# Kernel tuning notes

Measured on AMD Instinct MI355X. Metric: run time of the kernel, lower is better.

Reference implementation:

```python
import jax, jax.numpy as jnp
import numpy as np

N_FEAT = 512
N_HIDDEN = 512


def setup_inputs() -> dict:
    key = jax.random.key(0)
    ks = jax.random.split(key, 8)
    B, T, F = 32, 2048, N_FEAT
    H = N_HIDDEN
    s_ih = 1.0 / np.sqrt(H)
    X = jax.random.normal(ks[0], (B, T, F), dtype=jnp.float32)
    # PyTorch LSTMCell params: weight_ih [4H, F], weight_hh [4H, H], biases [4H]
    W_ih = jax.random.uniform(ks[1], (4 * H, F), minval=-s_ih, maxval=s_ih, dtype=jnp.float32)
    W_hh = jax.random.uniform(ks[2], (4 * H, H), minval=-s_ih, maxval=s_ih, dtype=jnp.float32)
    b_ih = jax.random.uniform(ks[3], (4 * H,), minval=-s_ih, maxval=s_ih, dtype=jnp.float32)
    b_hh = jax.random.uniform(ks[4], (4 * H,), minval=-s_ih, maxval=s_ih, dtype=jnp.float32)
    s_l = 1.0 / np.sqrt(F)
    W_hs = jax.random.uniform(ks[5], (F, F), minval=-s_l, maxval=s_l, dtype=jnp.float32)
    W_cs = jax.random.uniform(ks[6], (F, F), minval=-s_l, maxval=s_l, dtype=jnp.float32)
    return {"X": X, "W_ih": W_ih, "W_hh": W_hh, "b_ih": b_ih, "b_hh": b_hh,
            "W_hs": W_hs, "W_cs": W_cs}


def reference(X, W_ih, W_hh, b_ih, b_hh, W_hs, W_cs):
    B, T, F = X.shape
    H = W_hh.shape[1]

    def step(carry, xi):
        h, c = carry  # [B, H] each; note: h,c were linearly transformed last step
        gates = xi @ W_ih.T + b_ih + h @ W_hh.T + b_hh  # [B, 4H]
        i_g, f_g, g_g, o_g = jnp.split(gates, 4, axis=-1)  # PyTorch i,f,g,o order
        c_new = jax.nn.sigmoid(f_g) * c + jax.nn.sigmoid(i_g) * jnp.tanh(g_g)
        h_new = jax.nn.sigmoid(o_g) * jnp.tanh(c_new)
        h2 = h_new @ W_hs.T  # hs_state(h)
        c2 = c_new @ W_cs.T  # cs_state(c)
        att = jnp.tanh(h2 + c2)
        out = jnp.tanh(att + xi)
        return (h2, c2), out

    h0 = jnp.zeros((B, H), dtype=X.dtype)
    c0 = jnp.zeros((B, H), dtype=X.dtype)
    _, outs = jax.lax.scan(step, (h0, c0), jnp.transpose(X, (1, 0, 2)))  # [T, B, F]
    outs = jnp.transpose(outs, (1, 0, 2))  # [B, T, F]
    return X + jnp.tanh(outs)
```

## Files before the change

kernel.cpp:

```cpp
#include <hip/hip_runtime.h>

#define T_   2048
#define NWG  32

typedef float  float4v __attribute__((ext_vector_type(4)));
typedef float  float2v __attribute__((ext_vector_type(2)));
typedef short  short8v __attribute__((ext_vector_type(8)));
typedef short  short4v __attribute__((ext_vector_type(4)));
typedef unsigned uint4v __attribute__((ext_vector_type(4)));
typedef unsigned short ushort_t;

__device__ __forceinline__ ushort_t f2bf(float f) {
  union { float f; unsigned u; } v; v.f = f;
  unsigned r = (v.u + 0x7FFFu + ((v.u >> 16) & 1u)) >> 16;
  return (ushort_t)r;
}
__device__ __forceinline__ float bf2f(short s) {
  union { unsigned u; float f; } v; v.u = ((unsigned)(unsigned short)s) << 16;
  return v.f;
}
__device__ __forceinline__ float sigm(float x) {
  x = fmaxf(x, -30.f);
  return __fdividef(1.f, 1.f + __expf(-x));
}
__device__ __forceinline__ float tanh_(float x) {
  x = fminf(fmaxf(x, -15.f), 15.f);
  float e = __expf(2.f * x);
  return (e - 1.f) * __fdividef(1.f, e + 1.f);
}

__device__ __forceinline__ short8v ld_coh16(const ushort_t* p) {
  short8v r;
  asm volatile("global_load_dwordx4 %0, %1, off sc0 sc1" : "=v"(r) : "v"(p));
  return r;
}

__global__ void k_prep_w1(const float* __restrict__ Whh, const float* __restrict__ Whs,
                          ushort_t* __restrict__ w1) {
  int idx = blockIdx.x * 256 + threadIdx.x;
  if (idx >= 2048 * 512) return;
  int n = idx >> 9, k = idx & 511;
  const float* whr = Whh + (size_t)n * 512;
  const float* wsk = Whs + k;
  float s = 0.f;
  #pragma unroll 8
  for (int j = 0; j < 512; ++j) s += whr[j] * wsk[(size_t)j * 512];
  w1[idx] = f2bf(s);
}

__global__ void k_prep_misc(const float* __restrict__ Wih, const float* __restrict__ Wcs,
                            const float* __restrict__ Whs, const float* __restrict__ bih,
                            const float* __restrict__ bhh,
                            ushort_t* __restrict__ wih_bf, ushort_t* __restrict__ wcs_bf,
                            ushort_t* __restrict__ whs_bf, float* __restrict__ bias,
                            ushort_t* __restrict__ HN, ushort_t* __restrict__ CN,
                            int* __restrict__ flags) {
  const int total = 1048576 + 262144 + 262144 + 2048 + 16384 + 16384 + 512;
  for (int i = blockIdx.x * blockDim.x + threadIdx.x; i < total; i += gridDim.x * blockDim.x) {
    int r = i;
    if (r < 1048576) { wih_bf[r] = f2bf(Wih[r]); continue; }
    r -= 1048576;
    if (r < 262144)  { wcs_bf[r] = f2bf(Wcs[r]); continue; }
    r -= 262144;
    if (r < 262144)  { whs_bf[r] = f2bf(Whs[r]); continue; }
    r -= 262144;
    if (r < 2048)    { bias[r] = bih[r] + bhh[r]; continue; }
    r -= 2048;
    if (r < 16384)   { HN[3 * 16384 + r] = 0; continue; }
    r -= 16384;
    if (r < 16384)   { CN[3 * 16384 + r] = 0; continue; }
    r -= 16384;
    flags[r] = 0;
  }
}

__global__ __launch_bounds__(256) void k_gemm_g(
    const float* __restrict__ X, const ushort_t* __restrict__ wih,
    ushort_t* __restrict__ G) {
  const int bid = blockIdx.x;
  const int fb  = bid & 31;
  const int tg  = bid >> 5;
  const int wid = threadIdx.x >> 6;
  const int lane = threadIdx.x & 63;
  const int t   = tg * 4 + wid;
  const int ar  = lane & 15;
  const int ko  = (lane >> 4) << 3;

  float4v acc[2][4];
  #pragma unroll
  for (int mh = 0; mh < 2; ++mh)
    #pragma unroll
    for (int cg = 0; cg < 4; ++cg)
      acc[mh][cg] = float4v{0.f, 0.f, 0.f, 0.f};

  #pragma unroll 4
  for (int kk = 0; kk < 16; ++kk) {
    short8v a[2];
    #pragma unroll
    for (int mh = 0; mh < 2; ++mh) {
      const float* p = X + (size_t)(mh * 16 + ar) * (T_ * 512) + (size_t)t * 512 + kk * 32 + ko;
      float4v xa = *(const float4v*)(p);
      float4v xb = *(const float4v*)(p + 4);
      uint4v ua = __builtin_bit_cast(uint4v, xa);
      uint4v ub = __builtin_bit_cast(uint4v, xb);
      uint4v pk;
      pk[0] = __builtin_amdgcn_perm(ua[1], ua[0], 0x07060302u);
      pk[1] = __builtin_amdgcn_perm(ua[3], ua[2], 0x07060302u);
      pk[2] = __builtin_amdgcn_perm(ub[1], ub[0], 0x07060302u);
      pk[3] = __builtin_amdgcn_perm(ub[3], ub[2], 0x07060302u);
      a[mh] = __builtin_bit_cast(short8v, pk);
    }
    #pragma unroll
    for (int cg = 0; cg < 4; ++cg) {
      short8v b = *(const short8v*)(wih + ((size_t)(cg * 512 + fb * 16 + ar)) * 512 + kk * 32 + ko);
      acc[0][cg] = __builtin_amdgcn_mfma_f32_16x16x32_bf16(a[0], b, acc[0][cg], 0, 0, 0);
      acc[1][cg] = __builtin_amdgcn_mfma_f32_16x16x32_bf16(a[1], b, acc[1][cg], 0, 0, 0);
    }
  }

  const size_t base = ((size_t)t * 32 + fb) * 2048;
  #pragma unroll
  for (int mh = 0; mh < 2; ++mh)
    #pragma unroll
    for (int cg = 0; cg < 4; ++cg) {
      short4v s;
      #pragma unroll
      for (int r = 0; r < 4; ++r) s[r] = (short)f2bf(acc[mh][cg][r]);
      *(short4v*)(G + base + cg * 512 + ar * 32 + mh * 16 + ((lane >> 4) << 2)) = s;
    }
}

__global__ __launch_bounds__(256, 1) void k_lstm_pre(
    const float* __restrict__ X,
    const ushort_t* __restrict__ w1,
    const ushort_t* __restrict__ wcs, const ushort_t* __restrict__ whs,
    const float* __restrict__ bias, const ushort_t* __restrict__ G,
    ushort_t* __restrict__ HN, ushort_t* __restrict__ CN,
    int* __restrict__ flags, float* __restrict__ out)
{
  const int fb   = blockIdx.x;
  const int tid  = threadIdx.x;
  const int wid  = tid >> 6;
  const int lane = tid & 63;
  const int mh   = wid & 1;
  const int ar   = lane & 15;
  const int ko   = (lane >> 4) << 3;

  __shared__ float s_tiles[12][16][20];

  const int eb  = tid >> 3;
  const int ejp = (tid & 7) * 2;
  const int emh = eb >> 4, ebr = eb & 15;
  float bI[2], bF[2], bG[2], bO[2];
  #pragma unroll
  for (int u = 0; u < 2; ++u) {
    bI[u] = bias[0 * 512 + fb * 16 + ejp + u];
    bF[u] = bias[1 * 512 + fb * 16 + ejp + u];
    bG[u] = bias[2 * 512 + fb * 16 + ejp + u];
    bO[u] = bias[3 * 512 + fb * 16 + ejp + u];
  }

  const int gtype0 = wid >> 1;
  const int gtype1 = 2 + (wid >> 1);

  short8v bw0[16], bw1[16], bw2[16];
  {
    const ushort_t* p0 = w1 + ((size_t)(gtype0 * 512 + fb * 16 + ar)) * 512 + ko;
    const ushort_t* p1 = w1 + ((size_t)(gtype1 * 512 + fb * 16 + ar)) * 512 + ko;
    const ushort_t* p2 = ((wid < 2) ? wcs : whs) + ((size_t)(fb * 16 + ar)) * 512 + ko;
    #pragma unroll
    for (int kk = 0; kk < 16; ++kk) {
      bw0[kk] = *(const short8v*)(p0 + (size_t)kk * 32);
      bw1[kk] = *(const short8v*)(p1 + (size_t)kk * 32);
      bw2[kk] = *(const short8v*)(p2 + (size_t)kk * 32);
    }
  }

  const int arow_x = mh * 16 + ar;
  const int t0 = wid, t1 = wid + 4, t2 = wid + 8;
  const int glo = ((lane >> 4) << 2) + mh * 16 + ar * 32;

  short4v gp0, gp1;
  {
    const ushort_t* gb = G + (size_t)fb * 2048 + glo;
    gp0 = *(const short4v*)(gb + gtype0 * 512);
    gp1 = *(const short4v*)(gb + gtype1 * 512);
  }

  for (int t = 0; t <= T_; ++t) {
    float2v xo2 = {0.f, 0.f};
    if (t > 0)
      xo2 = *(const float2v*)&X[(size_t)eb * (T_ * 512) + (size_t)(t - 1) * 512 + fb * 16 + ejp];

    if (t > 0) {
      while (true) {
        int v = (lane < NWG)
              ? __hip_atomic_load(flags + lane * 16, __ATOMIC_RELAXED, __HIP_MEMORY_SCOPE_AGENT)
              : t;
        if (__all(v >= t)) break;
      }
      __builtin_amdgcn_sched_barrier(0);
    }

    const int rs = (t + 3) & 3;
    const ushort_t* hb = HN + (size_t)rs * (32 * 512) + (size_t)arow_x * 512 + ko;
    short8v hfrag[16];
    #pragma unroll
    for (int kk = 0; kk < 16; ++kk)
      hfrag[kk] = ld_coh16(hb + (size_t)kk * 32);
    short8v cfrag[16];
    if (wid < 2) {
      const ushort_t* cb = CN + (size_t)rs * (32 * 512) + (size_t)arow_x * 512 + ko;
      #pragma unroll
      for (int kk = 0; kk < 16; ++kk)
        cfrag[kk] = ld_coh16(cb + (size_t)kk * 32);
    }

    float4v acc0, acc1, acc2;
    #pragma unroll
    for (int r = 0; r < 4; ++r) {
      acc0[r] = bf2f(gp0[r]);
      acc1[r] = bf2f(gp1[r]);
      acc2[r] = 0.f;
    }

    asm volatile("s_waitcnt vmcnt(0)" ::: "memory");
    __builtin_amdgcn_sched_barrier(0);

    #pragma unroll
    for (int kk = 0; kk < 16; ++kk) {
      acc0 = __builtin_amdgcn_mfma_f32_16x16x32_bf16(hfrag[kk], bw0[kk], acc0, 0, 0, 0);
      acc1 = __builtin_amdgcn_mfma_f32_16x16x32_bf16(hfrag[kk], bw1[kk], acc1, 0, 0, 0);
      short8v a2 = (wid < 2) ? cfrag[kk] : hfrag[kk];
      acc2 = __builtin_amdgcn_mfma_f32_16x16x32_bf16(a2, bw2[kk], acc2, 0, 0, 0);
    }

    __syncthreads();

    {
      const int rb = (lane >> 4) << 2, cc = lane & 15;
      #pragma unroll
      for (int r = 0; r < 4; ++r) {
        s_tiles[t0][rb + r][cc] = acc0[r];
        s_tiles[t1][rb + r][cc] = acc1[r];
        s_tiles[t2][rb + r][cc] = acc2[r];
      }
    }
    __syncthreads();

    if (t < T_) {
      unsigned hpk = 0, cpk = 0;
      #pragma unroll
      for (int u = 0; u < 2; ++u) {
        int j = ejp + u;
        float iv  = s_tiles[0 + emh][ebr][j] + bI[u];
        float fv  = s_tiles[2 + emh][ebr][j] + bF[u];
        float gv  = s_tiles[4 + emh][ebr][j] + bG[u];
        float ov  = s_tiles[6 + emh][ebr][j] + bO[u];
        float c2p = s_tiles[8 + emh][ebr][j];
        float cnv = sigm(fv) * c2p + sigm(iv) * tanh_(gv);
        float hnv = sigm(ov) * tanh_(cnv);
        hpk |= ((unsigned)f2bf(hnv)) << (16 * u);
        cpk |= ((unsigned)f2bf(cnv)) << (16 * u);
      }
      size_t uso = (size_t)(t & 3) * (32 * 512) + (size_t)eb * 512 + fb * 16 + ejp;
      __hip_atomic_store((unsigned*)(HN + uso), hpk,
                         __ATOMIC_RELAXED, __HIP_MEMORY_SCOPE_AGENT);
      __hip_atomic_store((unsigned*)(CN + uso), cpk,
                         __ATOMIC_RELAXED, __HIP_MEMORY_SCOPE_AGENT);
    }
    __syncthreads();
    if (t < T_ && tid == 0)
      __hip_atomic_store(flags + fb * 16, t + 1, __ATOMIC_RELAXED, __HIP_MEMORY_SCOPE_AGENT);

    if (t + 1 < T_) {
      const ushort_t* gb = G + ((size_t)((t + 1) * 32 + fb)) * 2048 + glo;
      gp0 = *(const short4v*)(gb + gtype0 * 512);
      gp1 = *(const short4v*)(gb + gtype1 * 512);
    }

    if (t > 0) {
      float ov2[2];
      #pragma unroll
      for (int u = 0; u < 2; ++u) {
        int j = ejp + u;
        float c2p = s_tiles[8 + emh][ebr][j];
        float h2p = s_tiles[10 + emh][ebr][j];
        float att = tanh_(h2p + c2p);
        float xo  = (u ? xo2[1] : xo2[0]);
        float o1  = tanh_(att + xo);
        ov2[u] = xo + tanh_(o1);
      }
      float2v o2; o2[0] = ov2[0]; o2[1] = ov2[1];
      *(float2v*)&out[(size_t)eb * (T_ * 512) + (size_t)(t - 1) * 512 + fb * 16 + ejp] = o2;
    }
  }
}

__global__ __launch_bounds__(256, 1) void k_lstm_fb(
    const float* __restrict__ X,
    const ushort_t* __restrict__ w1, const ushort_t* __restrict__ wih,
    const ushort_t* __restrict__ wcs, const ushort_t* __restrict__ whs,
    const float* __restrict__ bias,
    ushort_t* __restrict__ HN, ushort_t* __restrict__ CN,
    int* __restrict__ flags, float* __restrict__ out)
{
  const int fb   = blockIdx.x;
  const int tid  = threadIdx.x;
  const int wid  = tid >> 6;
  const int lane = tid & 63;
  const int mh   = wid & 1;
  const int ar   = lane & 15;
  const int ko   = (lane >> 4) << 3;

  __shared__ float s_tiles[12][16][20];

  const int eb  = tid >> 3;
  const int ejp = (tid & 7) * 2;
  const int emh = eb >> 4, ebr = eb & 15;
  float bI[2], bF[2], bG[2], bO[2];
  #pragma unroll
  for (int u = 0; u < 2; ++u) {
    bI[u] = bias[0 * 512 + fb * 16 + ejp + u];
    bF[u] = bias[1 * 512 + fb * 16 + ejp + u];
    bG[u] = bias[2 * 512 + fb * 16 + ejp + u];
    bO[u] = bias[3 * 512 + fb * 16 + ejp + u];
  }

  const int gtype0 = wid >> 1;
  const int gtype1 = 2 + (wid >> 1);

  short8v bw0[16], bw1[16], bw2[16];
  {
    const ushort_t* p0 = w1 + ((size_t)(gtype0 * 512 + fb * 16 + ar)) * 512 + ko;
    const ushort_t* p1 = w1 + ((size_t)(gtype1 * 512 + fb * 16 + ar)) * 512 + ko;
    const ushort_t* p2 = ((wid < 2) ? wcs : whs) + ((size_t)(fb * 16 + ar)) * 512 + ko;
    #pragma unroll
    for (int kk = 0; kk < 16; ++kk) {
      bw0[kk] = *(const short8v*)(p0 + (size_t)kk * 32);
      bw1[kk] = *(const short8v*)(p1 + (size_t)kk * 32);
      bw2[kk] = *(const short8v*)(p2 + (size_t)kk * 32);
    }
  }

  const ushort_t* bx0_ = wih + ((size_t)(gtype0 * 512 + fb * 16 + ar)) * 512 + ko;
  const ushort_t* bx1_ = wih + ((size_t)(gtype1 * 512 + fb * 16 + ar)) * 512 + ko;
  const int arow_x = mh * 16 + ar;
  const int t0 = wid, t1 = wid + 4, t2 = wid + 8;

  for (int t = 0; t <= T_; ++t) {
    float4v acc0 = {0.f, 0.f, 0.f, 0.f};
    float4v acc1 = acc0, acc2 = acc0;

    float2v xo2 = {0.f, 0.f};
    if (t > 0)
      xo2 = *(const float2v*)&X[(size_t)eb * (T_ * 512) + (size_t)(t - 1) * 512 + fb * 16 + ejp];

    if (t < T_) {
      const float* xrow = X + (size_t)arow_x * (T_ * 512) + (size_t)t * 512 + ko;
      const ushort_t* bx0 = bx0_;
      const ushort_t* bx1 = bx1_;
      asm volatile("" : "+v"(bx0), "+v"(bx1));
      #pragma unroll
      for (int kk = 0; kk < 16; ++kk) {
        const float* p = xrow + kk * 32;
        float4v xa = *(const float4v*)(p);
        float4v xb = *(const float4v*)(p + 4);
        uint4v ua = __builtin_bit_cast(uint4v, xa);
        uint4v ub = __builtin_bit_cast(uint4v, xb);
        uint4v pk;
        pk[0] = __builtin_amdgcn_perm(ua[1], ua[0], 0x07060302u);
        pk[1] = __builtin_amdgcn_perm(ua[3], ua[2], 0x07060302u);
        pk[2] = __builtin_amdgcn_perm(ub[1], ub[0], 0x07060302u);
        pk[3] = __builtin_amdgcn_perm(ub[3], ub[2], 0x07060302u);
        short8v a = __builtin_bit_cast(short8v, pk);
        short8v b0 = *(const short8v*)(bx0 + (size_t)kk * 32);
        short8v b1 = *(const short8v*)(bx1 + (size_t)kk * 32);
        acc0 = __builtin_amdgcn_mfma_f32_16x16x32_bf16(a, b0, acc0, 0, 0, 0);
        acc1 = __builtin_amdgcn_mfma_f32_16x16x32_bf16(a, b1, acc1, 0, 0, 0);
      }
    }

    if (t > 0) {
      while (true) {
        int v = (lane < NWG)
              ? __hip_atomic_load(flags + lane * 16, __ATOMIC_RELAXED, __HIP_MEMORY_SCOPE_AGENT)
              : t;
        if (__all(v >= t)) break;
      }
      __builtin_amdgcn_sched_barrier(0);
    }

    const int rs = (t + 3) & 3;
    const ushort_t* hb = HN + (size_t)rs * (32 * 512) + (size_t)arow_x * 512 + ko;
    short8v hfrag[16];
    #pragma unroll
    for (int kk = 0; kk < 16; ++kk)
      hfrag[kk] = ld_coh16(hb + (size_t)kk * 32);
    short8v cfrag[16];
    if (wid < 2) {
      const ushort_t* cb = CN + (size_t)rs * (32 * 512) + (size_t)arow_x * 512 + ko;
      #pragma unroll
      for (int kk = 0; kk < 16; ++kk)
        cfrag[kk] = ld_coh16(cb + (size_t)kk * 32);
    }
    asm volatile("s_waitcnt vmcnt(0)" ::: "memory");
    __builtin_amdgcn_sched_barrier(0);

    #pragma unroll
    for (int kk = 0; kk < 16; ++kk) {
      acc0 = __builtin_amdgcn_mfma_f32_16x16x32_bf16(hfrag[kk], bw0[kk], acc0, 0, 0, 0);
      acc1 = __builtin_amdgcn_mfma_f32_16x16x32_bf16(hfrag[kk], bw1[kk], acc1, 0, 0, 0);
      short8v a2 = (wid < 2) ? cfrag[kk] : hfrag[kk];
      acc2 = __builtin_amdgcn_mfma_f32_16x16x32_bf16(a2, bw2[kk], acc2, 0, 0, 0);
    }

    __syncthreads();

    {
      const int rb = (lane >> 4) << 2, cc = lane & 15;
      #pragma unroll
      for (int r = 0; r < 4; ++r) {
        s_tiles[t0][rb + r][cc] = acc0[r];
        s_tiles[t1][rb + r][cc] = acc1[r];
        s_tiles[t2][rb + r][cc] = acc2[r];
      }
    }
    __syncthreads();

    if (t < T_) {
      unsigned hpk = 0, cpk = 0;
      #pragma unroll
      for (int u = 0; u < 2; ++u) {
        int j = ejp + u;
        float iv  = s_tiles[0 + emh][ebr][j] + bI[u];
        float fv  = s_tiles[2 + emh][ebr][j] + bF[u];
        float gv  = s_tiles[4 + emh][ebr][j] + bG[u];
        float ov  = s_tiles[6 + emh][ebr][j] + bO[u];
        float c2p = s_tiles[8 + emh][ebr][j];
        float cnv = sigm(fv) * c2p + sigm(iv) * tanh_(gv);
        float hnv = sigm(ov) * tanh_(cnv);
        hpk |= ((unsigned)f2bf(hnv)) << (16 * u);
        cpk |= ((unsigned)f2bf(cnv)) << (16 * u);
      }
      size_t uso = (size_t)(t & 3) * (32 * 512) + (size_t)eb * 512 + fb * 16 + ejp;
      __hip_atomic_store((unsigned*)(HN + uso), hpk,
                         __ATOMIC_RELAXED, __HIP_MEMORY_SCOPE_AGENT);
      __hip_atomic_store((unsigned*)(CN + uso), cpk,
                         __ATOMIC_RELAXED, __HIP_MEMORY_SCOPE_AGENT);
    }
    __syncthreads();
    if (t < T_ && tid == 0)
      __hip_atomic_store(flags + fb * 16, t + 1, __ATOMIC_RELAXED, __HIP_MEMORY_SCOPE_AGENT);

    if (t > 0) {
      float ov2[2];
      #pragma unroll
      for (int u = 0; u < 2; ++u) {
        int j = ejp + u;
        float c2p = s_tiles[8 + emh][ebr][j];
        float h2p = s_tiles[10 + emh][ebr][j];
        float att = tanh_(h2p + c2p);
        float xo  = (u ? xo2[1] : xo2[0]);
        float o1  = tanh_(att + xo);
        ov2[u] = xo + tanh_(o1);
      }
      float2v o2; o2[0] = ov2[0]; o2[1] = ov2[1];
      *(float2v*)&out[(size_t)eb * (T_ * 512) + (size_t)(t - 1) * 512 + fb * 16 + ejp] = o2;
    }
  }
}

extern "C" void kernel_launch(void* const* d_in, const int* in_sizes, int n_in,
                              void* d_out, int out_size, void* d_ws, size_t ws_size,
                              hipStream_t stream) {
  const float* X   = (const float*)d_in[0];
  const float* Wih = (const float*)d_in[1];
  const float* Whh = (const float*)d_in[2];
  const float* bih = (const float*)d_in[3];
  const float* bhh = (const float*)d_in[4];
  const float* Whs = (const float*)d_in[5];
  const float* Wcs = (const float*)d_in[6];

  char* ws = (char*)d_ws;
  ushort_t* w1_bf  = (ushort_t*)(ws + 0);
  ushort_t* wih_bf = (ushort_t*)(ws + 2097152);
  ushort_t* wcs_bf = (ushort_t*)(ws + 4194304);
  ushort_t* whs_bf = (ushort_t*)(ws + 4718592);
  float*    bias   = (float*)   (ws + 5242880);
  ushort_t* HN     = (ushort_t*)(ws + 5251072);
  ushort_t* CN     = (ushort_t*)(ws + 5382144);
  int*      flags  = (int*)     (ws + 5513216);
  ushort_t* G      = (ushort_t*)(ws + 5515264);
  if (ws_size < (size_t)5515264) return;
  const bool pre = ws_size >= (size_t)5515264 + (size_t)268435456;

  k_prep_w1<<<4096, 256, 0, stream>>>(Whh, Whs, w1_bf);
  k_prep_misc<<<2048, 256, 0, stream>>>(Wih, Wcs, Whs, bih, bhh,
                                        wih_bf, wcs_bf, whs_bf, bias, HN, CN, flags);
  if (pre) {
    k_gemm_g<<<16384, 256, 0, stream>>>(X, wih_bf, G);
    k_lstm_pre<<<NWG, 256, 0, stream>>>(X, w1_bf, wcs_bf, whs_bf, bias, G,
                                        HN, CN, flags, (float*)d_out);
  } else {
    k_lstm_fb<<<NWG, 256, 0, stream>>>(X, w1_bf, wih_bf, wcs_bf, whs_bf, bias,
                                       HN, CN, flags, (float*)d_out);
  }
}
```

Measured before the change: 11.45 ms.

## Double-buffer LDS tiles and replace block barrier with per-wave counter signaling

The shared-memory gate tiles are double-buffered by step parity. This removes two __syncthreads per timestep, and the output epilogue for step t-2 moves into the window before the MFMAs so it overlaps the recurrent-state load latency. The per-workgroup flag written by thread 0 after a block barrier becomes an atomic counter that each wave increments once its own h/c stores have drained. Consumers wait for 4*t arrivals. This shortens the critical path between steps, at the cost of more atomics and an extra epilogue after the loop.

```diff
diff --git a/kernel.cpp b/kernel.cpp
--- a/kernel.cpp
+++ b/kernel.cpp
@@ -54,7 +54,7 @@
                             ushort_t* __restrict__ wih_bf, ushort_t* __restrict__ wcs_bf,
                             ushort_t* __restrict__ whs_bf, float* __restrict__ bias,
                             ushort_t* __restrict__ HN, ushort_t* __restrict__ CN,
-                            int* __restrict__ flags) {
+                            int* __restrict__ cnt) {
   const int total = 1048576 + 262144 + 262144 + 2048 + 16384 + 16384 + 512;
   for (int i = blockIdx.x * blockDim.x + threadIdx.x; i < total; i += gridDim.x * blockDim.x) {
     int r = i;
@@ -70,7 +70,7 @@
     r -= 16384;
     if (r < 16384)   { CN[3 * 16384 + r] = 0; continue; }
     r -= 16384;
-    flags[r] = 0;
+    cnt[r] = 0;
   }
 }
 
@@ -136,7 +136,7 @@
     const ushort_t* __restrict__ wcs, const ushort_t* __restrict__ whs,
     const float* __restrict__ bias, const ushort_t* __restrict__ G,
     ushort_t* __restrict__ HN, ushort_t* __restrict__ CN,
-    int* __restrict__ flags, float* __restrict__ out)
+    int* __restrict__ cnt, float* __restrict__ out)
 {
   const int fb   = blockIdx.x;
   const int tid  = threadIdx.x;
@@ -146,7 +146,7 @@
   const int ar   = lane & 15;
   const int ko   = (lane >> 4) << 3;
 
-  __shared__ float s_tiles[12][16][20];
+  __shared__ float s_tiles[2][12][16][20];
 
   const int eb  = tid >> 3;
   const int ejp = (tid & 7) * 2;
@@ -189,15 +189,16 @@
 
   for (int t = 0; t <= T_; ++t) {
     float2v xo2 = {0.f, 0.f};
-    if (t > 0)
-      xo2 = *(const float2v*)&X[(size_t)eb * (T_ * 512) + (size_t)(t - 1) * 512 + fb * 16 + ejp];
+    if (t >= 2)
+      xo2 = *(const float2v*)&X[(size_t)eb * (T_ * 512) + (size_t)(t - 2) * 512 + fb * 16 + ejp];
 
     if (t > 0) {
+      const int thr = t << 2;
       while (true) {
         int v = (lane < NWG)
-              ? __hip_atomic_load(flags + lane * 16, __ATOMIC_RELAXED, __HIP_MEMORY_SCOPE_AGENT)
-              : t;
-        if (__all(v >= t)) break;
+              ? __hip_atomic_load(cnt + lane * 16, __ATOMIC_RELAXED, __HIP_MEMORY_SCOPE_AGENT)
+              : thr;
+        if (__all(v >= thr)) break;
       }
       __builtin_amdgcn_sched_barrier(0);
     }
@@ -215,6 +216,7 @@
       for (int kk = 0; kk < 16; ++kk)
         cfrag[kk] = ld_coh16(cb + (size_t)kk * 32);
     }
+    __builtin_amdgcn_sched_barrier(0);
 
     float4v acc0, acc1, acc2;
     #pragma unroll
@@ -222,6 +224,20 @@
       acc0[r] = bf2f(gp0[r]);
       acc1[r] = bf2f(gp1[r]);
       acc2[r] = 0.f;
+    }
+    float ov2[2];
+    if (t >= 2) {
+      const int p = (t - 1) & 1;
+      #pragma unroll
+      for (int u = 0; u < 2; ++u) {
+        int j = ejp + u;
+        float c2p = s_tiles[p][8 + emh][ebr][j];
+        float h2p = s_tiles[p][10 + emh][ebr][j];
+        float att = tanh_(h2p + c2p);
+        float xo  = (u ? xo2[1] : xo2[0]);
+        float o1  = tanh_(att + xo);
+        ov2[u] = xo + tanh_(o1);
+      }
     }
 
     asm volatile("s_waitcnt vmcnt(0)" ::: "memory");
@@ -235,15 +251,14 @@
       acc2 = __builtin_amdgcn_mfma_f32_16x16x32_bf16(a2, bw2[kk], acc2, 0, 0, 0);
     }
 
-    __syncthreads();
-
+    const int pb = t & 1;
     {
       const int rb = (lane >> 4) << 2, cc = lane & 15;
       #pragma unroll
       for (int r = 0; r < 4; ++r) {
-        s_tiles[t0][rb + r][cc] = acc0[r];
-        s_tiles[t1][rb + r][cc] = acc1[r];
-        s_tiles[t2][rb + r][cc] = acc2[r];
+        s_tiles[pb][t0][rb + r][cc] = acc0[r];
+        s_tiles[pb][t1][rb + r][cc] = acc1[r];
+        s_tiles[pb][t2][rb + r][cc] = acc2[r];
       }
     }
     __syncthreads();
@@ -253,11 +268,11 @@
       #pragma unroll
       for (int u = 0; u < 2; ++u) {
         int j = ejp + u;
-        float iv  = s_tiles[0 + emh][ebr][j] + bI[u];
-        float fv  = s_tiles[2 + emh][ebr][j] + bF[u];
-        float gv  = s_tiles[4 + emh][ebr][j] + bG[u];
-        float ov  = s_tiles[6 + emh][ebr][j] + bO[u];
-        float c2p = s_tiles[8 + emh][ebr][j];
+        float iv  = s_tiles[pb][0 + emh][ebr][j] + bI[u];
+        float fv  = s_tiles[pb][2 + emh][ebr][j] + bF[u];
+        float gv  = s_tiles[pb][4 + emh][ebr][j] + bG[u];
+        float ov  = s_tiles[pb][6 + emh][ebr][j] + bO[u];
+        float c2p = s_tiles[pb][8 + emh][ebr][j];
         float cnv = sigm(fv) * c2p + sigm(iv) * tanh_(gv);
         float hnv = sigm(ov) * tanh_(cnv);
         hpk |= ((unsigned)f2bf(hnv)) << (16 * u);
@@ -268,32 +283,39 @@
                          __ATOMIC_RELAXED, __HIP_MEMORY_SCOPE_AGENT);
       __hip_atomic_store((unsigned*)(CN + uso), cpk,
                          __ATOMIC_RELAXED, __HIP_MEMORY_SCOPE_AGENT);
-    }
-    __syncthreads();
-    if (t < T_ && tid == 0)
-      __hip_atomic_store(flags + fb * 16, t + 1, __ATOMIC_RELAXED, __HIP_MEMORY_SCOPE_AGENT);
+      asm volatile("s_waitcnt vmcnt(0)" ::: "memory");
+      if ((tid & 63) == 0)
+        __hip_atomic_fetch_add(cnt + fb * 16, 1, __ATOMIC_RELAXED, __HIP_MEMORY_SCOPE_AGENT);
+    }
+
+    if (t >= 2) {
+      float2v o2; o2[0] = ov2[0]; o2[1] = ov2[1];
+      *(float2v*)&out[(size_t)eb * (T_ * 512) + (size_t)(t - 2) * 512 + fb * 16 + ejp] = o2;
+    }
 
     if (t + 1 < T_) {
       const ushort_t* gb = G + ((size_t)((t + 1) * 32 + fb)) * 2048 + glo;
       gp0 = *(const short4v*)(gb + gtype0 * 512);
       gp1 = *(const short4v*)(gb + gtype1 * 512);
     }
-
-    if (t > 0) {
-      float ov2[2];
-      #pragma unroll
-      for (int u = 0; u < 2; ++u) {
-        int j = ejp + u;
-        float c2p = s_tiles[8 + emh][ebr][j];
-        float h2p = s_tiles[10 + emh][ebr][j];
-        float att = tanh_(h2p + c2p);
-        float xo  = (u ? xo2[1] : xo2[0]);
-        float o1  = tanh_(att + xo);
-        ov2[u] = xo + tanh_(o1);
-      }
-      float2v o2; o2[0] = ov2[0]; o2[1] = ov2[1];
-      *(float2v*)&out[(size_t)eb * (T_ * 512) + (size_t)(t - 1) * 512 + fb * 16 + ejp] = o2;
-    }
+  }
+
+  {
+    const int p = T_ & 1;
+    float2v xo2 = *(const float2v*)&X[(size_t)eb * (T_ * 512) + (size_t)(T_ - 1) * 512 + fb * 16 + ejp];
+    float ov2[2];
+    #pragma unroll
+    for (int u = 0; u < 2; ++u) {
+      int j = ejp + u;
+      float c2p = s_tiles[p][8 + emh][ebr][j];
+      float h2p = s_tiles[p][10 + emh][ebr][j];
+      float att = tanh_(h2p + c2p);
+      float xo  = (u ? xo2[1] : xo2[0]);
+      float o1  = tanh_(att + xo);
+      ov2[u] = xo + tanh_(o1);
+    }
+    float2v o2; o2[0] = ov2[0]; o2[1] = ov2[1];
+    *(float2v*)&out[(size_t)eb * (T_ * 512) + (size_t)(T_ - 1) * 512 + fb * 16 + ejp] = o2;
   }
 }
 
@@ -490,20 +512,20 @@
   float*    bias   = (float*)   (ws + 5242880);
   ushort_t* HN     = (ushort_t*)(ws + 5251072);
   ushort_t* CN     = (ushort_t*)(ws + 5382144);
-  int*      flags  = (int*)     (ws + 5513216);
+  int*      cnt    = (int*)     (ws + 5513216);
   ushort_t* G      = (ushort_t*)(ws + 5515264);
   if (ws_size < (size_t)5515264) return;
   const bool pre = ws_size >= (size_t)5515264 + (size_t)268435456;
 
   k_prep_w1<<<4096, 256, 0, stream>>>(Whh, Whs, w1_bf);
   k_prep_misc<<<2048, 256, 0, stream>>>(Wih, Wcs, Whs, bih, bhh,
-                                        wih_bf, wcs_bf, whs_bf, bias, HN, CN, flags);
+                                        wih_bf, wcs_bf, whs_bf, bias, HN, CN, cnt);
   if (pre) {
     k_gemm_g<<<16384, 256, 0, stream>>>(X, wih_bf, G);
     k_lstm_pre<<<NWG, 256, 0, stream>>>(X, w1_bf, wcs_bf, whs_bf, bias, G,
-                                        HN, CN, flags, (float*)d_out);
+                                        HN, CN, cnt, (float*)d_out);
   } else {
     k_lstm_fb<<<NWG, 256, 0, stream>>>(X, w1_bf, wih_bf, wcs_bf, whs_bf, bias,
-                                       HN, CN, flags, (float*)d_out);
-  }
-}
+                                       HN, CN, cnt, (float*)d_out);
+  }
+}
```

After: 14.19 ms. 1.24x slower.

## Fuse input-projection GEMM into recurrent kernel with per-timestep-group readiness counters

Applied to the files above, without the earlier changes.

Merges the standalone input-gate GEMM kernel and the persistent LSTM recurrence kernel into one launch. The first 32 blocks run the recurrence, and the remaining blocks compute G tiles and bump a per-timestep-group counter. The recurrence spins on that counter before reading each group of four timesteps. This overlaps the large GEMM with the serial recurrence instead of running them back to back. The cost is atomic loads and stores for G, extra spin-waits, and a dependence on the 32 recurrence blocks being scheduled first and staying co-resident.

```diff
diff --git a/kernel.cpp b/kernel.cpp
--- a/kernel.cpp
+++ b/kernel.cpp
@@ -9,6 +9,7 @@
 typedef short  short4v __attribute__((ext_vector_type(4)));
 typedef unsigned uint4v __attribute__((ext_vector_type(4)));
 typedef unsigned short ushort_t;
+typedef unsigned long long ull_t;
 
 __device__ __forceinline__ ushort_t f2bf(float f) {
   union { float f; unsigned u; } v; v.f = f;
@@ -54,8 +55,8 @@
                             ushort_t* __restrict__ wih_bf, ushort_t* __restrict__ wcs_bf,
                             ushort_t* __restrict__ whs_bf, float* __restrict__ bias,
                             ushort_t* __restrict__ HN, ushort_t* __restrict__ CN,
-                            int* __restrict__ flags) {
-  const int total = 1048576 + 262144 + 262144 + 2048 + 16384 + 16384 + 512;
+                            int* __restrict__ flags, int* __restrict__ gcnt) {
+  const int total = 1048576 + 262144 + 262144 + 2048 + 16384 + 16384 + 512 + 8192;
   for (int i = blockIdx.x * blockDim.x + threadIdx.x; i < total; i += gridDim.x * blockDim.x) {
     int r = i;
     if (r < 1048576) { wih_bf[r] = f2bf(Wih[r]); continue; }
@@ -70,81 +71,84 @@
     r -= 16384;
     if (r < 16384)   { CN[3 * 16384 + r] = 0; continue; }
     r -= 16384;
-    flags[r] = 0;
-  }
-}
-
-__global__ __launch_bounds__(256) void k_gemm_g(
-    const float* __restrict__ X, const ushort_t* __restrict__ wih,
-    ushort_t* __restrict__ G) {
-  const int bid = blockIdx.x;
-  const int fb  = bid & 31;
-  const int tg  = bid >> 5;
-  const int wid = threadIdx.x >> 6;
-  const int lane = threadIdx.x & 63;
-  const int t   = tg * 4 + wid;
-  const int ar  = lane & 15;
-  const int ko  = (lane >> 4) << 3;
-
-  float4v acc[2][4];
-  #pragma unroll
-  for (int mh = 0; mh < 2; ++mh)
-    #pragma unroll
-    for (int cg = 0; cg < 4; ++cg)
-      acc[mh][cg] = float4v{0.f, 0.f, 0.f, 0.f};
-
-  #pragma unroll 4
-  for (int kk = 0; kk < 16; ++kk) {
-    short8v a[2];
-    #pragma unroll
-    for (int mh = 0; mh < 2; ++mh) {
-      const float* p = X + (size_t)(mh * 16 + ar) * (T_ * 512) + (size_t)t * 512 + kk * 32 + ko;
-      float4v xa = *(const float4v*)(p);
-      float4v xb = *(const float4v*)(p + 4);
-      uint4v ua = __builtin_bit_cast(uint4v, xa);
-      uint4v ub = __builtin_bit_cast(uint4v, xb);
-      uint4v pk;
-      pk[0] = __builtin_amdgcn_perm(ua[1], ua[0], 0x07060302u);
-      pk[1] = __builtin_amdgcn_perm(ua[3], ua[2], 0x07060302u);
-      pk[2] = __builtin_amdgcn_perm(ub[1], ub[0], 0x07060302u);
-      pk[3] = __builtin_amdgcn_perm(ub[3], ub[2], 0x07060302u);
-      a[mh] = __builtin_bit_cast(short8v, pk);
-    }
-    #pragma unroll
-    for (int cg = 0; cg < 4; ++cg) {
-      short8v b = *(const short8v*)(wih + ((size_t)(cg * 512 + fb * 16 + ar)) * 512 + kk * 32 + ko);
-      acc[0][cg] = __builtin_amdgcn_mfma_f32_16x16x32_bf16(a[0], b, acc[0][cg], 0, 0, 0);
-      acc[1][cg] = __builtin_amdgcn_mfma_f32_16x16x32_bf16(a[1], b, acc[1][cg], 0, 0, 0);
-    }
-  }
-
-  const size_t base = ((size_t)t * 32 + fb) * 2048;
-  #pragma unroll
-  for (int mh = 0; mh < 2; ++mh)
-    #pragma unroll
-    for (int cg = 0; cg < 4; ++cg) {
-      short4v s;
-      #pragma unroll
-      for (int r = 0; r < 4; ++r) s[r] = (short)f2bf(acc[mh][cg][r]);
-      *(short4v*)(G + base + cg * 512 + ar * 32 + mh * 16 + ((lane >> 4) << 2)) = s;
-    }
-}
-
-__global__ __launch_bounds__(256, 1) void k_lstm_pre(
+    if (r < 512)     { flags[r] = 0; continue; }
+    r -= 512;
+    gcnt[r] = 0;
+  }
+}
+
+__global__ __launch_bounds__(256, 1) void k_fused(
     const float* __restrict__ X,
-    const ushort_t* __restrict__ w1,
+    const ushort_t* __restrict__ w1, const ushort_t* __restrict__ wih,
     const ushort_t* __restrict__ wcs, const ushort_t* __restrict__ whs,
-    const float* __restrict__ bias, const ushort_t* __restrict__ G,
+    const float* __restrict__ bias, ushort_t* __restrict__ G,
     ushort_t* __restrict__ HN, ushort_t* __restrict__ CN,
-    int* __restrict__ flags, float* __restrict__ out)
+    int* __restrict__ flags, int* __restrict__ gcnt, float* __restrict__ out)
 {
-  const int fb   = blockIdx.x;
   const int tid  = threadIdx.x;
   const int wid  = tid >> 6;
   const int lane = tid & 63;
-  const int mh   = wid & 1;
   const int ar   = lane & 15;
   const int ko   = (lane >> 4) << 3;
+
+  if (blockIdx.x >= 32) {
+    const int gbid = blockIdx.x - 32;
+    const int fb  = gbid & 31;
+    const int tg  = gbid >> 5;
+    const int t   = tg * 4 + wid;
+
+    float4v acc[2][4];
+    #pragma unroll
+    for (int mh = 0; mh < 2; ++mh)
+      #pragma unroll
+      for (int cg = 0; cg < 4; ++cg)
+        acc[mh][cg] = float4v{0.f, 0.f, 0.f, 0.f};
+
+    #pragma unroll 4
+    for (int kk = 0; kk < 16; ++kk) {
+      short8v a[2];
+      #pragma unroll
+      for (int mh = 0; mh < 2; ++mh) {
+        const float* p = X + (size_t)(mh * 16 + ar) * (T_ * 512) + (size_t)t * 512 + kk * 32 + ko;
+        float4v xa = *(const float4v*)(p);
+        float4v xb = *(const float4v*)(p + 4);
+        uint4v ua = __builtin_bit_cast(uint4v, xa);
+        uint4v ub = __builtin_bit_cast(uint4v, xb);
+        uint4v pk;
+        pk[0] = __builtin_amdgcn_perm(ua[1], ua[0], 0x07060302u);
+        pk[1] = __builtin_amdgcn_perm(ua[3], ua[2], 0x07060302u);
+        pk[2] = __builtin_amdgcn_perm(ub[1], ub[0], 0x07060302u);
+        pk[3] = __builtin_amdgcn_perm(ub[3], ub[2], 0x07060302u);
+        a[mh] = __builtin_bit_cast(short8v, pk);
+      }
+      #pragma unroll
+      for (int cg = 0; cg < 4; ++cg) {
+        short8v b = *(const short8v*)(wih + ((size_t)(cg * 512 + fb * 16 + ar)) * 512 + kk * 32 + ko);
+        acc[0][cg] = __builtin_amdgcn_mfma_f32_16x16x32_bf16(a[0], b, acc[0][cg], 0, 0, 0);
+        acc[1][cg] = __builtin_amdgcn_mfma_f32_16x16x32_bf16(a[1], b, acc[1][cg], 0, 0, 0);
+      }
+    }
+
+    const size_t base = ((size_t)t * 32 + fb) * 2048;
+    #pragma unroll
+    for (int mh = 0; mh < 2; ++mh)
+      #pragma unroll
+      for (int cg = 0; cg < 4; ++cg) {
+        short4v s;
+        #pragma unroll
+        for (int r = 0; r < 4; ++r) s[r] = (short)f2bf(acc[mh][cg][r]);
+        __hip_atomic_store(
+            (ull_t*)(G + base + cg * 512 + ar * 32 + mh * 16 + ((lane >> 4) << 2)),
+            __builtin_bit_cast(ull_t, s), __ATOMIC_RELAXED, __HIP_MEMORY_SCOPE_AGENT);
+      }
+    __syncthreads();
+    if (tid == 0)
+      __hip_atomic_fetch_add(gcnt + tg * 16, 1, __ATOMIC_RELAXED, __HIP_MEMORY_SCOPE_AGENT);
+    return;
+  }
+
+  const int fb = blockIdx.x;
+  const int mh = wid & 1;
 
   __shared__ float s_tiles[12][16][20];
 
@@ -182,9 +186,12 @@
 
   short4v gp0, gp1;
   {
+    while (__hip_atomic_load(gcnt, __ATOMIC_RELAXED, __HIP_MEMORY_SCOPE_AGENT) < 32) {}
     const ushort_t* gb = G + (size_t)fb * 2048 + glo;
-    gp0 = *(const short4v*)(gb + gtype0 * 512);
-    gp1 = *(const short4v*)(gb + gtype1 * 512);
+    gp0 = __builtin_bit_cast(short4v,
+        __hip_atomic_load((const ull_t*)(gb + gtype0 * 512), __ATOMIC_RELAXED, __HIP_MEMORY_SCOPE_AGENT));
+    gp1 = __builtin_bit_cast(short4v,
+        __hip_atomic_load((const ull_t*)(gb + gtype1 * 512), __ATOMIC_RELAXED, __HIP_MEMORY_SCOPE_AGENT));
   }
 
   for (int t = 0; t <= T_; ++t) {
@@ -274,9 +281,15 @@
       __hip_atomic_store(flags + fb * 16, t + 1, __ATOMIC_RELAXED, __HIP_MEMORY_SCOPE_AGENT);
 
     if (t + 1 < T_) {
+      if (((t + 1) & 3) == 0) {
+        const int* gq = gcnt + ((t + 1) >> 2) * 16;
+        while (__hip_atomic_load(gq, __ATOMIC_RELAXED, __HIP_MEMORY_SCOPE_AGENT) < 32) {}
+      }
       const ushort_t* gb = G + ((size_t)((t + 1) * 32 + fb)) * 2048 + glo;
-      gp0 = *(const short4v*)(gb + gtype0 * 512);
-      gp1 = *(const short4v*)(gb + gtype1 * 512);
+      gp0 = __builtin_bit_cast(short4v,
+          __hip_atomic_load((const ull_t*)(gb + gtype0 * 512), __ATOMIC_RELAXED, __HIP_MEMORY_SCOPE_AGENT));
+      gp1 = __builtin_bit_cast(short4v,
+          __hip_atomic_load((const ull_t*)(gb + gtype1 * 512), __ATOMIC_RELAXED, __HIP_MEMORY_SCOPE_AGENT));
     }
 
     if (t > 0) {
@@ -491,17 +504,17 @@
   ushort_t* HN     = (ushort_t*)(ws + 5251072);
   ushort_t* CN     = (ushort_t*)(ws + 5382144);
   int*      flags  = (int*)     (ws + 5513216);
-  ushort_t* G      = (ushort_t*)(ws + 5515264);
-  if (ws_size < (size_t)5515264) return;
-  const bool pre = ws_size >= (size_t)5515264 + (size_t)268435456;
+  int*      gcnt   = (int*)     (ws + 5515264);
+  ushort_t* G      = (ushort_t*)(ws + 5548032);
+  if (ws_size < (size_t)5548032) return;
+  const bool pre = ws_size >= (size_t)5548032 + (size_t)268435456;
 
   k_prep_w1<<<4096, 256, 0, stream>>>(Whh, Whs, w1_bf);
   k_prep_misc<<<2048, 256, 0, stream>>>(Wih, Wcs, Whs, bih, bhh,
-                                        wih_bf, wcs_bf, whs_bf, bias, HN, CN, flags);
+                                        wih_bf, wcs_bf, whs_bf, bias, HN, CN, flags, gcnt);
   if (pre) {
-    k_gemm_g<<<16384, 256, 0, stream>>>(X, wih_bf, G);
-    k_lstm_pre<<<NWG, 256, 0, stream>>>(X, w1_bf, wcs_bf, whs_bf, bias, G,
-                                        HN, CN, flags, (float*)d_out);
+    k_fused<<<32 + 16384, 256, 0, stream>>>(X, w1_bf, wih_bf, wcs_bf, whs_bf, bias, G,
+                                            HN, CN, flags, gcnt, (float*)d_out);
   } else {
     k_lstm_fb<<<NWG, 256, 0, stream>>>(X, w1_bf, wih_bf, wcs_bf, whs_bf, bias,
                                        HN, CN, flags, (float*)d_out);
```

Measured after the change: 10.81 ms. 1.06x faster.
